# Kernel optimization log

Measured on AMD Instinct MI355X. Metric: run time of the kernel, lower is better.

## Reference

```python
import jax, jax.numpy as jnp
import numpy as np

B, T, D = 8, 4096, 64

def setup_inputs() -> dict:
    key = jax.random.key(0)
    k1, k2 = jax.random.split(key)
    inputs = jax.random.normal(k1, (B, T, D), dtype=jnp.float32)
    # keras 'random_normal' initializer: stddev 0.05
    W = jax.random.normal(k2, (D, D), dtype=jnp.float32) * 0.05
    return {"inputs": inputs, "W": W}

def reference(inputs, W):
    # q = inputs @ W               : [B,T,D]
    # a = q @ inputs^T             : [B,T,T] (no scaling, bias b unused in original)
    # out = softmax(a, -1) @ inputs: [B,T,D]
    q = jnp.einsum('btd,de->bte', inputs, W)
    scores = jnp.einsum('btd,bsd->bts', q, inputs)
    attn = jax.nn.softmax(scores, axis=-1)
    return jnp.einsum('bts,bsd->btd', attn, inputs)
```

## Files before the change

### kernel.cpp

```cpp
#include <hip/hip_runtime.h>

typedef _Float16 f16;
typedef _Float16 f16x8 __attribute__((ext_vector_type(8)));
typedef __bf16 bf16x8 __attribute__((ext_vector_type(8)));
typedef __bf16 bf16x4 __attribute__((ext_vector_type(4)));
typedef float floatx4 __attribute__((ext_vector_type(4)));
typedef unsigned short u16;
typedef unsigned int u32;

#define B_N   8
#define T_SEQ 4096
#define DIM   64
#define QT    64
#define KT    256
#define NIT   (T_SEQ / KT)
#define PSTR2 264
#define XSTR  72
#define LOG2E 1.44269504f
#define FRAG  512

#if __has_builtin(__builtin_amdgcn_exp2f)
#define EXP2(x) __builtin_amdgcn_exp2f(x)
#else
#define EXP2(x) exp2f(x)
#endif

__launch_bounds__(256, 2)
__global__ void prep_kernel(const float* __restrict__ X, const float* __restrict__ W,
                            u16* __restrict__ Kswz, u16* __restrict__ Qswz,
                            u16* __restrict__ Vswz) {
  __shared__ __attribute__((aligned(16))) u16 Xs[DIM * XSTR];
  __shared__ __attribute__((aligned(16))) u16 Wt[DIM * XSTR];
  __shared__ __attribute__((aligned(16))) u16 Qs[DIM * XSTR];
  const int tid = threadIdx.x;
  const int lane = tid & 63, w = tid >> 6, qd = lane >> 4, ln = lane & 15;
  const int b = blockIdx.y;
  const int t0 = blockIdx.x * 64;
  const long xbase = ((long)b * T_SEQ + t0) * DIM;

  {
    const int r = tid >> 2, c0 = (tid & 3) * 16;
    float v[16];
#pragma unroll
    for (int i = 0; i < 4; i++)
      *(float4*)&v[i * 4] = *(const float4*)(X + xbase + (long)r * DIM + c0 + i * 4);
    u16 h[16];
#pragma unroll
    for (int j = 0; j < 16; j++) h[j] = __builtin_bit_cast(u16, (f16)v[j]);
    *(uint4*)&Xs[r * XSTR + c0] = *(uint4*)&h[0];
    *(uint4*)&Xs[r * XSTR + c0 + 8] = *(uint4*)&h[8];
    float wv[16];
#pragma unroll
    for (int i = 0; i < 4; i++)
      *(float4*)&wv[i * 4] = *(const float4*)(W + r * DIM + c0 + i * 4);
#pragma unroll
    for (int j = 0; j < 16; j++) Wt[(c0 + j) * XSTR + r] = __builtin_bit_cast(u16, (f16)wv[j]);
  }
  __syncthreads();

  {
    const long R = (long)b * (T_SEQ / 16) + blockIdx.x * 4 + w;
#pragma unroll
    for (int ks = 0; ks < 2; ks++) {
      f16x8 kv = *(const f16x8*)&Xs[(w * 16 + ln) * XSTR + ks * 32 + qd * 8];
      *(f16x8*)(Kswz + (R * 2 + ks) * FRAG + lane * 8) = kv;
    }
  }

  {
    const int wq = w * 16;
    floatx4 acc[4];
#pragma unroll
    for (int ct = 0; ct < 4; ct++) acc[ct] = (floatx4)0.0f;
#pragma unroll
    for (int ks = 0; ks < 2; ks++) {
      f16x8 aX = *(const f16x8*)&Xs[(wq + ln) * XSTR + ks * 32 + qd * 8];
#pragma unroll
      for (int ct = 0; ct < 4; ct++) {
        f16x8 bW = *(const f16x8*)&Wt[(ct * 16 + ln) * XSTR + ks * 32 + qd * 8];
        acc[ct] = __builtin_amdgcn_mfma_f32_16x16x32_f16(aX, bW, acc[ct], 0, 0, 0);
      }
    }
#pragma unroll
    for (int ct = 0; ct < 4; ct++)
#pragma unroll
      for (int r = 0; r < 4; r++)
        Qs[(wq + qd * 4 + r) * XSTR + ct * 16 + ln] =
            __builtin_bit_cast(u16, (f16)(acc[ct][r] * LOG2E));
  }

  {
    const long Cb = (long)b * 4 + w;
    const int J0 = blockIdx.x * 2;
#pragma unroll
    for (int J = 0; J < 2; J++) {
      bf16x8 vv;
#pragma unroll
      for (int j = 0; j < 8; j++) {
        f16 hv = __builtin_bit_cast(f16, Xs[(J * 32 + qd * 8 + j) * XSTR + w * 16 + ln]);
        vv[j] = (__bf16)(float)hv;
      }
      *(bf16x8*)(Vswz + (Cb * (T_SEQ / 32) + J0 + J) * FRAG + lane * 8) = vv;
    }
  }

  {
    const long R = (long)b * (T_SEQ / 16) + blockIdx.x * 4 + w;
#pragma unroll
    for (int ks = 0; ks < 2; ks++) {
      f16x8 qv = *(const f16x8*)&Qs[(w * 16 + ln) * XSTR + ks * 32 + qd * 8];
      *(f16x8*)(Qswz + (R * 2 + ks) * FRAG + lane * 8) = qv;
    }
  }
}

__launch_bounds__(512, 4)
__global__ void attn_kernel(const u16* __restrict__ Kswz, const u16* __restrict__ Qswz,
                            const u16* __restrict__ Vswz, float* __restrict__ out) {
  __shared__ __attribute__((aligned(16))) u16 Ps[QT * PSTR2];
  __shared__ float lpart[8][QT];

  float* Opart = (float*)Ps;

  const int tid = threadIdx.x;
  const int lane = tid & 63;
  const int w = tid >> 6;
  const int qd = lane >> 4;
  const int ln = lane & 15;
  const int dq = w & 3;
  const int kh = w >> 2;
  const int bid = blockIdx.x;
  const int b = bid & 7;
  const int q0 = (bid >> 3) * QT;
  const long bbase = (long)b * T_SEQ * DIM;

  const u16* pKf = Kswz + ((long)b * (T_SEQ / 16) + w * 2) * 2 * FRAG + lane * 8;
  const u16* pVf = Vswz + ((long)(b * 4 + dq)) * (T_SEQ / 32) * FRAG + lane * 8;

  f16x8 aQ[4][2];
#pragma unroll
  for (int rb = 0; rb < 4; rb++)
#pragma unroll
    for (int ks = 0; ks < 2; ks++)
      aQ[rb][ks] = *(const f16x8*)(Qswz +
          (((long)b * (T_SEQ / 16) + (q0 >> 4) + rb) * 2 + ks) * FRAG + lane * 8);

  floatx4 O[4];
  float lacc[4] = {0.f, 0.f, 0.f, 0.f};
#pragma unroll
  for (int rb = 0; rb < 4; rb++) O[rb] = (floatx4)0.0f;

#pragma unroll 1
  for (int kt = 0; kt < NIT; kt++) {
    f16x8 bK[2][2];
#pragma unroll
    for (int ct = 0; ct < 2; ct++)
#pragma unroll
      for (int ks = 0; ks < 2; ks++)
        bK[ct][ks] = *(const f16x8*)(pKf + ((long)(kt * 16 + ct) * 2 + ks) * FRAG);

    floatx4 St[2][4];
#pragma unroll
    for (int ct = 0; ct < 2; ct++)
#pragma unroll
      for (int rb = 0; rb < 4; rb++) St[ct][rb] = (floatx4)0.0f;
#pragma unroll
    for (int ks = 0; ks < 2; ks++)
#pragma unroll
      for (int ct = 0; ct < 2; ct++)
#pragma unroll
        for (int rb = 0; rb < 4; rb++)
          St[ct][rb] = __builtin_amdgcn_mfma_f32_16x16x32_f16(bK[ct][ks], aQ[rb][ks], St[ct][rb], 0, 0, 0);

#pragma unroll
    for (int rb = 0; rb < 4; rb++)
#pragma unroll
      for (int ct = 0; ct < 2; ct++) {
        bf16x4 pk;
        float ps = 0.f;
#pragma unroll
        for (int r = 0; r < 4; r++) {
          float p = EXP2(St[ct][rb][r]);
          ps += p;
          pk[r] = (__bf16)p;
        }
        lacc[rb] += ps;
        *(uint2*)&Ps[(rb * 16 + ln) * PSTR2 + w * 32 + ct * 16 + qd * 4] =
            __builtin_bit_cast(uint2, pk);
      }

    bf16x8 bV[4];
#pragma unroll
    for (int ks = 0; ks < 4; ks++)
      bV[ks] = *(const bf16x8*)(pVf + (long)(kt * 8 + kh * 4 + ks) * FRAG);

    __syncthreads();

#pragma unroll
    for (int rb = 0; rb < 4; rb++)
#pragma unroll
      for (int ks = 0; ks < 4; ks++) {
        bf16x8 aP = *(const bf16x8*)&Ps[(rb * 16 + ln) * PSTR2 + kh * 128 + ks * 32 + qd * 8];
        O[rb] = __builtin_amdgcn_mfma_f32_16x16x32_bf16(aP, bV[ks], O[rb], 0, 0, 0);
      }

    __syncthreads();
  }

#pragma unroll
  for (int rb = 0; rb < 4; rb++) {
    float v = lacc[rb];
    v += __shfl_xor(v, 16, 64);
    v += __shfl_xor(v, 32, 64);
    if (qd == 0) lpart[w][rb * 16 + ln] = v;
  }

#pragma unroll 1
  for (int g = 0; g < 2; g++) {
    __syncthreads();
#pragma unroll
    for (int h = 0; h < 2; h++) {
      const int rb = g * 2 + h;
#pragma unroll
      for (int r = 0; r < 4; r++)
        Opart[(kh * 32 + h * 16 + qd * 4 + r) * 68 + dq * 16 + ln] = O[rb][r];
    }
    __syncthreads();
    const int ql = tid >> 4;
    const int d0 = (tid & 15) * 4;
    const int q = g * 32 + ql;
    float4 s0 = *(const float4*)&Opart[(0 * 32 + ql) * 68 + d0];
    float4 s1 = *(const float4*)&Opart[(1 * 32 + ql) * 68 + d0];
    float l = 0.f;
#pragma unroll
    for (int ww = 0; ww < 8; ww++) l += lpart[ww][q];
    float inv = 1.0f / l;
    float4 o;
    o.x = (s0.x + s1.x) * inv;
    o.y = (s0.y + s1.y) * inv;
    o.z = (s0.z + s1.z) * inv;
    o.w = (s0.w + s1.w) * inv;
    *(float4*)(out + bbase + (long)(q0 + q) * DIM + d0) = o;
  }
}

extern "C" void kernel_launch(void* const* d_in, const int* in_sizes, int n_in,
                              void* d_out, int out_size, void* d_ws, size_t ws_size,
                              hipStream_t stream) {
  const float* X = (const float*)d_in[0];
  const float* W = (const float*)d_in[1];
  float* out = (float*)d_out;
  const size_t SZ = (size_t)B_N * T_SEQ * DIM * 2;
  u16* Kswz = (u16*)d_ws;
  u16* Qswz = (u16*)((char*)d_ws + SZ);
  u16* Vswz = (u16*)((char*)d_ws + 2 * SZ);
  prep_kernel<<<dim3(T_SEQ / 64, B_N), 256, 0, stream>>>(X, W, Kswz, Qswz, Vswz);
  attn_kernel<<<dim3(B_N * (T_SEQ / QT)), 512, 0, stream>>>(Kswz, Qswz, Vswz, out);
}
```

Baseline: 105.7 us.

## Fuse Q projection into attention kernel and keep P in registers via lane shuffles

Moves the Q = X·W projection out of the prep kernel and into the attention kernel, computing it transposed per wave from the K fragments, which removes the Q workspace buffer and its write/read traffic. The attention loop is reorganized so each wave owns a 32-query half and a quarter of the key stream. The softmax probabilities are transposed in registers with cross-lane shuffles rather than staged through shared memory, which eliminates both per-iteration __syncthreads and the LDS round trip. In exchange it adds shuffle instructions per iteration, redundant W loads and conversions per block, and a final reduction across four waves instead of two.

```diff
diff --git a/kernel.cpp b/kernel.cpp
--- a/kernel.cpp
+++ b/kernel.cpp
@@ -3,7 +3,6 @@
 typedef _Float16 f16;
 typedef _Float16 f16x8 __attribute__((ext_vector_type(8)));
 typedef __bf16 bf16x8 __attribute__((ext_vector_type(8)));
-typedef __bf16 bf16x4 __attribute__((ext_vector_type(4)));
 typedef float floatx4 __attribute__((ext_vector_type(4)));
 typedef unsigned short u16;
 typedef unsigned int u32;
@@ -11,13 +10,10 @@
 #define B_N   8
 #define T_SEQ 4096
 #define DIM   64
-#define QT    64
-#define KT    256
-#define NIT   (T_SEQ / KT)
-#define PSTR2 264
+#define NIT   32
+#define FRAG  512
 #define XSTR  72
 #define LOG2E 1.44269504f
-#define FRAG  512
 
 #if __has_builtin(__builtin_amdgcn_exp2f)
 #define EXP2(x) __builtin_amdgcn_exp2f(x)
@@ -25,18 +21,46 @@
 #define EXP2(x) exp2f(x)
 #endif
 
+__device__ __forceinline__ uint4 xpose(uint2 p0, uint2 p1, int qd, int ln) {
+  const int pos = qd & 1;
+  u32 mx = pos ? p1.x : p0.x, my = pos ? p1.y : p0.y;
+  u32 ox = pos ? p0.x : p1.x, oy = pos ? p0.y : p1.y;
+  u32 tx = (u32)__shfl_xor((int)ox, 16, 64);
+  u32 ty = (u32)__shfl_xor((int)oy, 16, 64);
+  u32 lox = pos ? tx : mx, loy = pos ? ty : my;
+  u32 hix = pos ? mx : tx, hiy = pos ? my : ty;
+  const int src = ((2 * pos + (qd >> 1)) << 4) | ln;
+  uint4 r;
+  r.x = (u32)__shfl((int)lox, src, 64);
+  r.y = (u32)__shfl((int)loy, src, 64);
+  r.z = (u32)__shfl((int)hix, src, 64);
+  r.w = (u32)__shfl((int)hiy, src, 64);
+  return r;
+}
+
+__device__ __forceinline__ uint2 pack_bf4(floatx4 v) {
+  __bf16 b0 = (__bf16)v[0], b1 = (__bf16)v[1], b2 = (__bf16)v[2], b3 = (__bf16)v[3];
+  uint2 r;
+  r.x = ((u32)__builtin_bit_cast(u16, b1) << 16) | __builtin_bit_cast(u16, b0);
+  r.y = ((u32)__builtin_bit_cast(u16, b3) << 16) | __builtin_bit_cast(u16, b2);
+  return r;
+}
+__device__ __forceinline__ uint2 pack_f16x4(floatx4 v, float sc) {
+  f16 b0 = (f16)(v[0] * sc), b1 = (f16)(v[1] * sc), b2 = (f16)(v[2] * sc), b3 = (f16)(v[3] * sc);
+  uint2 r;
+  r.x = ((u32)__builtin_bit_cast(u16, b1) << 16) | __builtin_bit_cast(u16, b0);
+  r.y = ((u32)__builtin_bit_cast(u16, b3) << 16) | __builtin_bit_cast(u16, b2);
+  return r;
+}
+
 __launch_bounds__(256, 2)
-__global__ void prep_kernel(const float* __restrict__ X, const float* __restrict__ W,
-                            u16* __restrict__ Kswz, u16* __restrict__ Qswz,
-                            u16* __restrict__ Vswz) {
+__global__ void prep_kernel(const float* __restrict__ X,
+                            u16* __restrict__ Kswz, u16* __restrict__ Vswz) {
   __shared__ __attribute__((aligned(16))) u16 Xs[DIM * XSTR];
-  __shared__ __attribute__((aligned(16))) u16 Wt[DIM * XSTR];
-  __shared__ __attribute__((aligned(16))) u16 Qs[DIM * XSTR];
   const int tid = threadIdx.x;
   const int lane = tid & 63, w = tid >> 6, qd = lane >> 4, ln = lane & 15;
-  const int b = blockIdx.y;
-  const int t0 = blockIdx.x * 64;
-  const long xbase = ((long)b * T_SEQ + t0) * DIM;
+  const int b = blockIdx.y, tx = blockIdx.x;
+  const long xbase = ((long)b * T_SEQ + tx * 64) * DIM;
 
   {
     const int r = tid >> 2, c0 = (tid & 3) * 16;
@@ -49,49 +73,19 @@
     for (int j = 0; j < 16; j++) h[j] = __builtin_bit_cast(u16, (f16)v[j]);
     *(uint4*)&Xs[r * XSTR + c0] = *(uint4*)&h[0];
     *(uint4*)&Xs[r * XSTR + c0 + 8] = *(uint4*)&h[8];
-    float wv[16];
-#pragma unroll
-    for (int i = 0; i < 4; i++)
-      *(float4*)&wv[i * 4] = *(const float4*)(W + r * DIM + c0 + i * 4);
-#pragma unroll
-    for (int j = 0; j < 16; j++) Wt[(c0 + j) * XSTR + r] = __builtin_bit_cast(u16, (f16)wv[j]);
   }
   __syncthreads();
 
   {
-    const long R = (long)b * (T_SEQ / 16) + blockIdx.x * 4 + w;
+    const long R = (long)b * (T_SEQ / 16) + tx * 4 + w;
 #pragma unroll
     for (int ks = 0; ks < 2; ks++) {
       f16x8 kv = *(const f16x8*)&Xs[(w * 16 + ln) * XSTR + ks * 32 + qd * 8];
       *(f16x8*)(Kswz + (R * 2 + ks) * FRAG + lane * 8) = kv;
     }
   }
-
-  {
-    const int wq = w * 16;
-    floatx4 acc[4];
-#pragma unroll
-    for (int ct = 0; ct < 4; ct++) acc[ct] = (floatx4)0.0f;
-#pragma unroll
-    for (int ks = 0; ks < 2; ks++) {
-      f16x8 aX = *(const f16x8*)&Xs[(wq + ln) * XSTR + ks * 32 + qd * 8];
-#pragma unroll
-      for (int ct = 0; ct < 4; ct++) {
-        f16x8 bW = *(const f16x8*)&Wt[(ct * 16 + ln) * XSTR + ks * 32 + qd * 8];
-        acc[ct] = __builtin_amdgcn_mfma_f32_16x16x32_f16(aX, bW, acc[ct], 0, 0, 0);
-      }
-    }
-#pragma unroll
-    for (int ct = 0; ct < 4; ct++)
-#pragma unroll
-      for (int r = 0; r < 4; r++)
-        Qs[(wq + qd * 4 + r) * XSTR + ct * 16 + ln] =
-            __builtin_bit_cast(u16, (f16)(acc[ct][r] * LOG2E));
-  }
-
   {
     const long Cb = (long)b * 4 + w;
-    const int J0 = blockIdx.x * 2;
 #pragma unroll
     for (int J = 0; J < 2; J++) {
       bf16x8 vv;
@@ -100,115 +94,123 @@
         f16 hv = __builtin_bit_cast(f16, Xs[(J * 32 + qd * 8 + j) * XSTR + w * 16 + ln]);
         vv[j] = (__bf16)(float)hv;
       }
-      *(bf16x8*)(Vswz + (Cb * (T_SEQ / 32) + J0 + J) * FRAG + lane * 8) = vv;
-    }
-  }
-
-  {
-    const long R = (long)b * (T_SEQ / 16) + blockIdx.x * 4 + w;
-#pragma unroll
-    for (int ks = 0; ks < 2; ks++) {
-      f16x8 qv = *(const f16x8*)&Qs[(w * 16 + ln) * XSTR + ks * 32 + qd * 8];
-      *(f16x8*)(Qswz + (R * 2 + ks) * FRAG + lane * 8) = qv;
+      *(bf16x8*)(Vswz + (Cb * (T_SEQ / 32) + tx * 2 + J) * FRAG + lane * 8) = vv;
     }
   }
 }
 
 __launch_bounds__(512, 4)
-__global__ void attn_kernel(const u16* __restrict__ Kswz, const u16* __restrict__ Qswz,
-                            const u16* __restrict__ Vswz, float* __restrict__ out) {
-  __shared__ __attribute__((aligned(16))) u16 Ps[QT * PSTR2];
-  __shared__ float lpart[8][QT];
-
-  float* Opart = (float*)Ps;
+__global__ void attn_kernel(const u16* __restrict__ Kswz, const u16* __restrict__ Vswz,
+                            const float* __restrict__ W, float* __restrict__ out) {
+  __shared__ __attribute__((aligned(16))) float Opart[8][16][68];
+  __shared__ float lpart[8][32];
 
   const int tid = threadIdx.x;
-  const int lane = tid & 63;
-  const int w = tid >> 6;
-  const int qd = lane >> 4;
-  const int ln = lane & 15;
-  const int dq = w & 3;
-  const int kh = w >> 2;
+  const int lane = tid & 63, w = tid >> 6, qd = lane >> 4, ln = lane & 15;
+  const int h = w >> 2;
+  const int s = w & 3;
   const int bid = blockIdx.x;
   const int b = bid & 7;
-  const int q0 = (bid >> 3) * QT;
+  const int q0 = (bid >> 3) * 64;
   const long bbase = (long)b * T_SEQ * DIM;
-
-  const u16* pKf = Kswz + ((long)b * (T_SEQ / 16) + w * 2) * 2 * FRAG + lane * 8;
-  const u16* pVf = Vswz + ((long)(b * 4 + dq)) * (T_SEQ / 32) * FRAG + lane * 8;
-
-  f16x8 aQ[4][2];
-#pragma unroll
-  for (int rb = 0; rb < 4; rb++)
+  const long RB = (long)b * (T_SEQ / 16);
+
+  f16x8 bXq[2][2];
+#pragma unroll
+  for (int rb = 0; rb < 2; rb++)
 #pragma unroll
     for (int ks = 0; ks < 2; ks++)
-      aQ[rb][ks] = *(const f16x8*)(Qswz +
-          (((long)b * (T_SEQ / 16) + (q0 >> 4) + rb) * 2 + ks) * FRAG + lane * 8);
-
-  floatx4 O[4];
-  float lacc[4] = {0.f, 0.f, 0.f, 0.f};
-#pragma unroll
-  for (int rb = 0; rb < 4; rb++) O[rb] = (floatx4)0.0f;
+      bXq[rb][ks] = *(const f16x8*)(Kswz +
+          ((RB + (q0 >> 4) + h * 2 + rb) * 2 + ks) * FRAG + lane * 8);
+
+  floatx4 accT[4][2];
+#pragma unroll
+  for (int eb = 0; eb < 4; eb++)
+#pragma unroll
+    for (int rb = 0; rb < 2; rb++) accT[eb][rb] = (floatx4)0.0f;
+#pragma unroll
+  for (int ks = 0; ks < 2; ks++)
+#pragma unroll
+    for (int eb = 0; eb < 4; eb++) {
+      f16 tw[8];
+#pragma unroll
+      for (int j = 0; j < 8; j++)
+        tw[j] = (f16)W[(ks * 32 + qd * 8 + j) * DIM + eb * 16 + ln];
+      f16x8 aW = *(const f16x8*)tw;
+#pragma unroll
+      for (int rb = 0; rb < 2; rb++)
+        accT[eb][rb] = __builtin_amdgcn_mfma_f32_16x16x32_f16(aW, bXq[rb][ks], accT[eb][rb], 0, 0, 0);
+    }
+
+  f16x8 bQ[2][2];
+#pragma unroll
+  for (int rb = 0; rb < 2; rb++)
+#pragma unroll
+    for (int ks = 0; ks < 2; ks++) {
+      uint2 p0 = pack_f16x4(accT[ks * 2 + 0][rb], LOG2E);
+      uint2 p1 = pack_f16x4(accT[ks * 2 + 1][rb], LOG2E);
+      uint4 t = xpose(p0, p1, qd, ln);
+      bQ[rb][ks] = __builtin_bit_cast(f16x8, t);
+    }
+
+  floatx4 O[4][2];
+  float lacc[2] = {0.f, 0.f};
+#pragma unroll
+  for (int db = 0; db < 4; db++)
+#pragma unroll
+    for (int rb = 0; rb < 2; rb++) O[db][rb] = (floatx4)0.0f;
+
+  const u16* pK = Kswz + (RB + s * 2) * 2 * FRAG + lane * 8;
+  const u16* pV = Vswz + ((long)(b * 4) * (T_SEQ / 32) + s) * FRAG + lane * 8;
 
 #pragma unroll 1
   for (int kt = 0; kt < NIT; kt++) {
-    f16x8 bK[2][2];
+    f16x8 kc[2][2];
 #pragma unroll
     for (int ct = 0; ct < 2; ct++)
 #pragma unroll
       for (int ks = 0; ks < 2; ks++)
-        bK[ct][ks] = *(const f16x8*)(pKf + ((long)(kt * 16 + ct) * 2 + ks) * FRAG);
-
-    floatx4 St[2][4];
+        kc[ct][ks] = *(const f16x8*)(pK + (long)(kt * 16 + ct * 2 + ks) * FRAG);
+    bf16x8 aV[4];
+#pragma unroll
+    for (int db = 0; db < 4; db++)
+      aV[db] = *(const bf16x8*)(pV + ((long)db * (T_SEQ / 32) + kt * 4) * FRAG);
+
+    floatx4 St[2][2];
 #pragma unroll
     for (int ct = 0; ct < 2; ct++)
 #pragma unroll
-      for (int rb = 0; rb < 4; rb++) St[ct][rb] = (floatx4)0.0f;
+      for (int rb = 0; rb < 2; rb++) St[ct][rb] = (floatx4)0.0f;
 #pragma unroll
     for (int ks = 0; ks < 2; ks++)
 #pragma unroll
       for (int ct = 0; ct < 2; ct++)
 #pragma unroll
-        for (int rb = 0; rb < 4; rb++)
-          St[ct][rb] = __builtin_amdgcn_mfma_f32_16x16x32_f16(bK[ct][ks], aQ[rb][ks], St[ct][rb], 0, 0, 0);
-
-#pragma unroll
-    for (int rb = 0; rb < 4; rb++)
-#pragma unroll
-      for (int ct = 0; ct < 2; ct++) {
-        bf16x4 pk;
-        float ps = 0.f;
-#pragma unroll
-        for (int r = 0; r < 4; r++) {
-          float p = EXP2(St[ct][rb][r]);
-          ps += p;
-          pk[r] = (__bf16)p;
-        }
-        lacc[rb] += ps;
-        *(uint2*)&Ps[(rb * 16 + ln) * PSTR2 + w * 32 + ct * 16 + qd * 4] =
-            __builtin_bit_cast(uint2, pk);
-      }
-
-    bf16x8 bV[4];
-#pragma unroll
-    for (int ks = 0; ks < 4; ks++)
-      bV[ks] = *(const bf16x8*)(pVf + (long)(kt * 8 + kh * 4 + ks) * FRAG);
-
-    __syncthreads();
-
-#pragma unroll
-    for (int rb = 0; rb < 4; rb++)
-#pragma unroll
-      for (int ks = 0; ks < 4; ks++) {
-        bf16x8 aP = *(const bf16x8*)&Ps[(rb * 16 + ln) * PSTR2 + kh * 128 + ks * 32 + qd * 8];
-        O[rb] = __builtin_amdgcn_mfma_f32_16x16x32_bf16(aP, bV[ks], O[rb], 0, 0, 0);
-      }
-
-    __syncthreads();
-  }
-
-#pragma unroll
-  for (int rb = 0; rb < 4; rb++) {
+        for (int rb = 0; rb < 2; rb++)
+          St[ct][rb] = __builtin_amdgcn_mfma_f32_16x16x32_f16(kc[ct][ks], bQ[rb][ks], St[ct][rb], 0, 0, 0);
+
+    bf16x8 bP[2];
+#pragma unroll
+    for (int rb = 0; rb < 2; rb++) {
+      floatx4 e0, e1;
+      float ps = 0.f;
+#pragma unroll
+      for (int r = 0; r < 4; r++) { e0[r] = EXP2(St[0][rb][r]); ps += e0[r]; }
+#pragma unroll
+      for (int r = 0; r < 4; r++) { e1[r] = EXP2(St[1][rb][r]); ps += e1[r]; }
+      lacc[rb] += ps;
+      bP[rb] = __builtin_bit_cast(bf16x8, xpose(pack_bf4(e0), pack_bf4(e1), qd, ln));
+    }
+
+#pragma unroll
+    for (int db = 0; db < 4; db++)
+#pragma unroll
+      for (int rb = 0; rb < 2; rb++)
+        O[db][rb] = __builtin_amdgcn_mfma_f32_16x16x32_bf16(aV[db], bP[rb], O[db][rb], 0, 0, 0);
+  }
+
+#pragma unroll
+  for (int rb = 0; rb < 2; rb++) {
     float v = lacc[rb];
     v += __shfl_xor(v, 16, 64);
     v += __shfl_xor(v, 32, 64);
@@ -216,31 +218,28 @@
   }
 
 #pragma unroll 1
-  for (int g = 0; g < 2; g++) {
+  for (int rb = 0; rb < 2; rb++) {
     __syncthreads();
 #pragma unroll
-    for (int h = 0; h < 2; h++) {
-      const int rb = g * 2 + h;
-#pragma unroll
-      for (int r = 0; r < 4; r++)
-        Opart[(kh * 32 + h * 16 + qd * 4 + r) * 68 + dq * 16 + ln] = O[rb][r];
-    }
+    for (int db = 0; db < 4; db++)
+      *(float4*)&Opart[w][ln][db * 16 + qd * 4] = __builtin_bit_cast(float4, O[db][rb]);
     __syncthreads();
-    const int ql = tid >> 4;
-    const int d0 = (tid & 15) * 4;
-    const int q = g * 32 + ql;
-    float4 s0 = *(const float4*)&Opart[(0 * 32 + ql) * 68 + d0];
-    float4 s1 = *(const float4*)&Opart[(1 * 32 + ql) * 68 + d0];
+    const int hh = tid >> 8;
+    const int ql = (tid >> 4) & 15;
+    const int d4 = tid & 15;
+    float4 a = {0.f, 0.f, 0.f, 0.f};
     float l = 0.f;
 #pragma unroll
-    for (int ww = 0; ww < 8; ww++) l += lpart[ww][q];
+    for (int ss = 0; ss < 4; ss++) {
+      const int ww = hh * 4 + ss;
+      float4 p = *(const float4*)&Opart[ww][ql][d4 * 4];
+      a.x += p.x; a.y += p.y; a.z += p.z; a.w += p.w;
+      l += lpart[ww][rb * 16 + ql];
+    }
     float inv = 1.0f / l;
     float4 o;
-    o.x = (s0.x + s1.x) * inv;
-    o.y = (s0.y + s1.y) * inv;
-    o.z = (s0.z + s1.z) * inv;
-    o.w = (s0.w + s1.w) * inv;
-    *(float4*)(out + bbase + (long)(q0 + q) * DIM + d0) = o;
+    o.x = a.x * inv; o.y = a.y * inv; o.z = a.z * inv; o.w = a.w * inv;
+    *(float4*)(out + bbase + (long)(q0 + hh * 32 + rb * 16 + ql) * DIM + d4 * 4) = o;
   }
 }
 
@@ -252,8 +251,7 @@
   float* out = (float*)d_out;
   const size_t SZ = (size_t)B_N * T_SEQ * DIM * 2;
   u16* Kswz = (u16*)d_ws;
-  u16* Qswz = (u16*)((char*)d_ws + SZ);
-  u16* Vswz = (u16*)((char*)d_ws + 2 * SZ);
-  prep_kernel<<<dim3(T_SEQ / 64, B_N), 256, 0, stream>>>(X, W, Kswz, Qswz, Vswz);
-  attn_kernel<<<dim3(B_N * (T_SEQ / QT)), 512, 0, stream>>>(Kswz, Qswz, Vswz, out);
-}
+  u16* Vswz = (u16*)((char*)d_ws + SZ);
+  prep_kernel<<<dim3(T_SEQ / 64, B_N), 256, 0, stream>>>(X, Kswz, Vswz);
+  attn_kernel<<<dim3(B_N * (T_SEQ / 64)), 512, 0, stream>>>(Kswz, Vswz, W, out);
+}
```

Result: slower. 125.5 us (+18.7%).
